# Performance work log

Hardware: AMD Instinct MI355X
Metric: run time of the kernel (lower is better)

Reference implementation:

```python
import jax, jax.numpy as jnp
import numpy as np

N_MEM = 50000
MATCH_THR2 = 0.01   # squared-distance match threshold (0.1 m)
EMA = 0.5           # EMA factor for matched-descriptor update
EPS = 1e-8


def _bilinear_depth(depth, uv):
    # depth: [H, W]; uv: [M, 2] pixel coords (u = x/col, v = y/row)
    H, W = depth.shape
    u = jnp.clip(uv[:, 0], 0.0, W - 1.001)
    v = jnp.clip(uv[:, 1], 0.0, H - 1.001)
    u0 = jnp.floor(u); v0 = jnp.floor(v)
    du = u - u0; dv = v - v0
    u0i = u0.astype(jnp.int32); v0i = v0.astype(jnp.int32)
    d00 = depth[v0i, u0i]
    d01 = depth[v0i, u0i + 1]
    d10 = depth[v0i + 1, u0i]
    d11 = depth[v0i + 1, u0i + 1]
    return d00 * (1 - du) * (1 - dv) + d01 * du * (1 - dv) + d10 * (1 - du) * dv + d11 * du * dv


def pix2world(points, depth_map, pose, K):
    # points [B,M,2], depth_map [B,1,H,W], pose [B,3,4] cam->world, K [B,3,3]
    d = jax.vmap(_bilinear_depth)(depth_map[:, 0], points)            # [B,M]
    pix = jnp.concatenate([points, jnp.ones_like(points[..., :1])], -1)  # [B,M,3]
    Kinv = jnp.linalg.inv(K)
    cam = jnp.einsum('bij,bmj->bmi', Kinv, pix) * d[..., None]        # [B,M,3]
    world = jnp.einsum('bij,bmj->bmi', pose[:, :, :3], cam) + pose[:, :, 3][:, None, :]
    valid = (d > 0) & jnp.isfinite(world).all(-1)                      # [B,M]
    return world, valid


def memory_write(pts, desc, valid, mem_pts, mem_desc, next_ptr):
    # pts [P,3], desc [P,D]; mem_pts [N,3], mem_desc [N,D]
    d2 = (jnp.sum(pts * pts, -1, keepdims=True)
          - 2.0 * pts @ mem_pts.T
          + jnp.sum(mem_pts * mem_pts, -1)[None, :])                  # [P,N]
    idx = jnp.argmin(d2, axis=1)                                       # [P]
    dmin = jnp.take_along_axis(d2, idx[:, None], axis=1)[:, 0]
    match = (dmin < MATCH_THR2) & valid
    n_match = match.sum()
    # returned descriptors come from the (non-differentiable) memory buffer;
    # unmatched entries return their own descriptor (cos=1 -> zero loss/grad)
    matched_desc = jax.lax.stop_gradient(jnp.where(match[:, None], mem_desc[idx], desc))
    # --- state update (buffers: no gradient) ---
    dsg = jax.lax.stop_gradient(desc)
    psg = jax.lax.stop_gradient(pts)
    unm = (~match) & valid
    slots = (next_ptr + jnp.cumsum(unm.astype(jnp.int32)) - 1) % N_MEM
    widx = jnp.where(unm, slots, idx)                                  # [P]
    old_pts = mem_pts[widx]; old_desc = mem_desc[widx]
    upd = old_desc * EMA + dsg * (1.0 - EMA)
    upd = upd / (jnp.linalg.norm(upd, axis=-1, keepdims=True) + EPS)
    new_desc_vals = jnp.where(match[:, None], upd, jnp.where(unm[:, None], dsg, old_desc))
    new_pts_vals = jnp.where(unm[:, None], psg, old_pts)
    new_mem_desc = mem_desc.at[widx].set(new_desc_vals)
    new_mem_pts = mem_pts.at[widx].set(new_pts_vals)
    return matched_desc, n_match, new_mem_pts, new_mem_desc


def setup_inputs() -> dict:
    key = jax.random.key(0)
    ks = jax.random.split(key, 8)
    B, M, D, H, W = 8, 512, 256, 480, 640
    points = jax.random.uniform(ks[0], (B, M, 2), jnp.float32) * jnp.array([W - 2.0, H - 2.0])
    depth_map = 0.5 + 4.5 * jax.random.uniform(ks[1], (B, 1, H, W), jnp.float32)
    # proper rotations via QR + small translations
    A = np.asarray(jax.random.normal(ks[2], (B, 3, 3)))
    Rs = np.stack([np.linalg.qr(A[b])[0] for b in range(B)]).astype(np.float32)
    t = np.asarray(jax.random.normal(ks[3], (B, 3, 1))) * 2.0
    pose = jnp.asarray(np.concatenate([Rs, t.astype(np.float32)], axis=2))  # [B,3,4]
    Kmat = jnp.broadcast_to(jnp.array([[320.0, 0.0, 320.0], [0.0, 320.0, 240.0], [0.0, 0.0, 1.0]], jnp.float32), (B, 3, 3))
    descriptors = jax.random.normal(ks[4], (B, M, D), jnp.float32)
    mem_pts = (jax.random.uniform(ks[5], (N_MEM, 3), jnp.float32) - 0.5) * 16.0
    mem_desc = jax.random.normal(ks[6], (N_MEM, D), jnp.float32)
    mem_desc = mem_desc / (jnp.linalg.norm(mem_desc, axis=-1, keepdims=True) + EPS)
    return {"points": points, "depth_map": depth_map, "pose": pose, "K": Kmat,
            "descriptors": descriptors, "mem_pts": mem_pts, "mem_desc": mem_desc,
            "next_ptr": 20000}


def reference(points, depth_map, pose, K, descriptors, mem_pts, mem_desc, next_ptr):
    world, valid = pix2world(points, depth_map, pose, K)               # [B,M,3], [B,M]
    P = world.shape[0] * world.shape[1]
    pts = world.reshape(P, 3)
    desc = descriptors.reshape(P, -1)
    vmask = valid.reshape(P)
    pts = jnp.where(vmask[:, None], pts, 1e6)   # invalid points never match
    matched_desc, n_match, new_mem_pts, new_mem_desc = memory_write(
        pts, desc, vmask, mem_pts, mem_desc, next_ptr)
    a = desc / jnp.maximum(jnp.linalg.norm(desc, axis=-1, keepdims=True), EPS)
    b = matched_desc / jnp.maximum(jnp.linalg.norm(matched_desc, axis=-1, keepdims=True), EPS)
    cos = jnp.sum(a * b, -1)                                           # [P]
    nv = jnp.maximum(vmask.sum(), 1)
    loss = 1.0 - jnp.sum(cos * vmask) / nv
    return loss, n_match, new_mem_pts, new_mem_desc
```

## Files before the change

### kernel.cpp

```cpp
#include <hip/hip_runtime.h>
#include <math.h>

#define N_MEM   50000
#define P_TOT   4096
#define DDIM    256
#define HDIM    480
#define WDIM    640
#define CHUNK   196
#define DISTB   1024
#define COPYB   512
#define THR2    0.01f
#define EPSF    1e-8f
typedef unsigned long long ull;

__device__ __forceinline__ unsigned fsort(float x) {
    unsigned b = __float_as_uint(x);
    return (b & 0x80000000u) ? ~b : (b | 0x80000000u);
}

__global__ void k_world(const float* __restrict__ points,
                        const float* __restrict__ depth,
                        const float* __restrict__ pose,
                        const float* __restrict__ Kmat,
                        float4* __restrict__ pts_out,
                        int* __restrict__ flags_out,
                        ull* __restrict__ minkey)
{
    int p = blockIdx.x * 256 + threadIdx.x;
    if (p >= P_TOT) return;
    minkey[p] = 0xFFFFFFFFFFFFFFFFULL;
    int b = p >> 9;
    const float* K = Kmat + b * 9;
    float a00=K[0],a01=K[1],a02=K[2],a10=K[3],a11=K[4],a12=K[5],a20=K[6],a21=K[7],a22=K[8];
    float det = a00*(a11*a22-a12*a21) - a01*(a10*a22-a12*a20) + a02*(a10*a21-a11*a20);
    float id = 1.0f/det;
    float i00=(a11*a22-a12*a21)*id, i01=(a02*a21-a01*a22)*id, i02=(a01*a12-a02*a11)*id;
    float i10=(a12*a20-a10*a22)*id, i11=(a00*a22-a02*a20)*id, i12=(a02*a10-a00*a12)*id;
    float i20=(a10*a21-a11*a20)*id, i21=(a01*a20-a00*a21)*id, i22=(a00*a11-a01*a10)*id;

    float u = points[p*2+0], v = points[p*2+1];
    float uc = fminf(fmaxf(u, 0.f), (float)WDIM - 1.001f);
    float vc = fminf(fmaxf(v, 0.f), (float)HDIM - 1.001f);
    float u0 = floorf(uc), v0 = floorf(vc);
    float du = uc - u0, dv = vc - v0;
    int u0i = (int)u0, v0i = (int)v0;
    const float* dm = depth + (size_t)b * HDIM * WDIM;
    float d00 = dm[v0i*WDIM + u0i];
    float d01 = dm[v0i*WDIM + u0i + 1];
    float d10 = dm[(v0i+1)*WDIM + u0i];
    float d11 = dm[(v0i+1)*WDIM + u0i + 1];
    float d = d00*(1.f-du)*(1.f-dv) + d01*du*(1.f-dv) + d10*(1.f-du)*dv + d11*du*dv;

    float cx = (i00*u + i01*v + i02) * d;
    float cy = (i10*u + i11*v + i12) * d;
    float cz = (i20*u + i21*v + i22) * d;
    const float* T = pose + b * 12;
    float wx = T[0]*cx + T[1]*cy + T[2]*cz  + T[3];
    float wy = T[4]*cx + T[5]*cy + T[6]*cz  + T[7];
    float wz = T[8]*cx + T[9]*cy + T[10]*cz + T[11];
    int val = (d > 0.f) && isfinite(wx) && isfinite(wy) && isfinite(wz);
    float4 o = val ? make_float4(wx, wy, wz, 0.f) : make_float4(1e6f, 1e6f, 1e6f, 0.f);
    pts_out[p] = o;
    flags_out[p] = val;
}

__global__ __launch_bounds__(256) void k_main(const float4* __restrict__ pts,
                                              const float* __restrict__ mem_pts,
                                              const float* __restrict__ mem_desc,
                                              ull* __restrict__ minkey,
                                              float* __restrict__ out_pts,
                                              float* __restrict__ out_desc)
{
    __shared__ float4 sm[CHUNK];
    int bid = blockIdx.x;
    int t = threadIdx.x;
    if (bid < DISTB) {
        int pb = bid >> 8;
        int ch = bid & 255;
        int j0 = ch * CHUNK;
        int cnt = min(CHUNK, N_MEM - j0);
        if (t < cnt) {
            float mx = mem_pts[(j0 + t) * 3 + 0];
            float my = mem_pts[(j0 + t) * 3 + 1];
            float mz = mem_pts[(j0 + t) * 3 + 2];
            sm[t] = make_float4(mx, my, mz, mx*mx + my*my + mz*mz);
        }
        __syncthreads();
        int p0 = pb * 1024 + t;
        float4 P0 = pts[p0], P1 = pts[p0+256], P2 = pts[p0+512], P3 = pts[p0+768];
        float pp0 = P0.x*P0.x + P0.y*P0.y + P0.z*P0.z;
        float pp1 = P1.x*P1.x + P1.y*P1.y + P1.z*P1.z;
        float pp2 = P2.x*P2.x + P2.y*P2.y + P2.z*P2.z;
        float pp3 = P3.x*P3.x + P3.y*P3.y + P3.z*P3.z;
        float bd0 = 3.4e38f, bd1 = 3.4e38f, bd2 = 3.4e38f, bd3 = 3.4e38f;
        int bi0 = 0, bi1 = 0, bi2 = 0, bi3 = 0;
        for (int j = 0; j < cnt; ++j) {
            float4 mv = sm[j];
            float dot0 = P0.x*mv.x + P0.y*mv.y + P0.z*mv.z;
            float dot1 = P1.x*mv.x + P1.y*mv.y + P1.z*mv.z;
            float dot2 = P2.x*mv.x + P2.y*mv.y + P2.z*mv.z;
            float dot3 = P3.x*mv.x + P3.y*mv.y + P3.z*mv.z;
            float d0 = pp0 - 2.f*dot0 + mv.w;
            float d1 = pp1 - 2.f*dot1 + mv.w;
            float d2 = pp2 - 2.f*dot2 + mv.w;
            float d3 = pp3 - 2.f*dot3 + mv.w;
            if (d0 < bd0) { bd0 = d0; bi0 = j0 + j; }
            if (d1 < bd1) { bd1 = d1; bi1 = j0 + j; }
            if (d2 < bd2) { bd2 = d2; bi2 = j0 + j; }
            if (d3 < bd3) { bd3 = d3; bi3 = j0 + j; }
        }
        atomicMin(&minkey[p0],       ((ull)fsort(bd0) << 32) | (unsigned)bi0);
        atomicMin(&minkey[p0 + 256], ((ull)fsort(bd1) << 32) | (unsigned)bi1);
        atomicMin(&minkey[p0 + 512], ((ull)fsort(bd2) << 32) | (unsigned)bi2);
        atomicMin(&minkey[p0 + 768], ((ull)fsort(bd3) << 32) | (unsigned)bi3);
    } else {
        const long tid = (long)(bid - DISTB) * 256 + t;
        const long stride = (long)COPYB * 256;
        const float2* ds = (const float2*)mem_desc;
        float2* dd = (float2*)out_desc;
        const long ND2 = (long)N_MEM * DDIM / 2;
        long k = tid * 4;
        const long stride4 = stride * 4;
        for (; k + 3 < ND2; k += stride4) {
            float2 a0 = ds[k+0], a1 = ds[k+1], a2 = ds[k+2], a3 = ds[k+3];
            dd[k+0] = a0; dd[k+1] = a1; dd[k+2] = a2; dd[k+3] = a3;
        }
        for (; k < ND2; ++k) dd[k] = ds[k];
        const float2* ps = (const float2*)mem_pts;
        float2* pd = (float2*)out_pts;
        for (long i = tid; i < (long)N_MEM * 3 / 2; i += stride) pd[i] = ps[i];
    }
}

__global__ __launch_bounds__(256) void k_scan(const ull* __restrict__ minkey,
                                              int* __restrict__ flags,
                                              const int* __restrict__ next_ptr,
                                              int* __restrict__ widx,
                                              int* __restrict__ winner,
                                              float* __restrict__ dout)
{
    __shared__ int su[256];
    __shared__ int smc[256];
    int t = threadIdx.x;
    int base = t * 16;
    const ull thr_key = ((ull)fsort(THR2)) << 32;
    int um[16], iv[16], wvv[16];
    int usum = 0, msum = 0;
    for (int k = 0; k < 16; k++) {
        ull key = minkey[base + k];
        int v = flags[base + k] & 1;
        int m = (key < thr_key) && v;
        int u = (!m) && v;
        iv[k] = (int)(key & 0xffffffffULL);
        um[k] = u; usum += u; msum += m;
        flags[base + k] = v | (m << 1) | (u << 2);
    }
    su[t] = usum; smc[t] = msum;
    __syncthreads();
    for (int off = 1; off < 256; off <<= 1) {
        int a = su[t], b = (t >= off) ? su[t - off] : 0;
        int c = smc[t], d = (t >= off) ? smc[t - off] : 0;
        __syncthreads();
        su[t] = a + b; smc[t] = c + d;
        __syncthreads();
    }
    int excl = su[t] - usum;
    int np_ = *next_ptr;
    int run = excl;
    for (int k = 0; k < 16; k++) {
        int wv;
        if (um[k]) { run += 1; wv = (np_ + run - 1) % N_MEM; }
        else       { wv = iv[k]; }
        widx[base + k] = wv;
        wvv[k] = wv;
        winner[wv] = -1;
    }
    __syncthreads();
    for (int k = 0; k < 16; k++)
        atomicMax(&winner[wvv[k]], base + k);
    if (t == 255) dout[1] = (float)smc[255];
}

__global__ __launch_bounds__(256) void k_scatloss(const int* __restrict__ widx,
                                                  const int* __restrict__ flags,
                                                  const int* __restrict__ winner,
                                                  const float* __restrict__ desc,
                                                  const float4* __restrict__ pts,
                                                  const float* __restrict__ mem_pts,
                                                  const float* __restrict__ mem_desc,
                                                  float* __restrict__ out_pts,
                                                  float* __restrict__ out_desc,
                                                  float* __restrict__ cos_ws)
{
    __shared__ float red[16];
    int p = blockIdx.x;
    int t = threadIdx.x;
    int f = flags[p];
    int v = f & 1, m = (f >> 1) & 1, u = (f >> 2) & 1;
    int wi = widx[p];
    int win = (winner[wi] == p);
    if (!m && !win) {
        if (t == 0) cos_ws[p] = v ? 1.f : 0.f;
        return;
    }
    float dsg = desc[p * DDIM + t];
    float old = mem_desc[(long)wi * DDIM + t];
    float val, cosv;
    if (m) {
        float up = old * 0.5f + dsg * 0.5f;
        float sdd = dsg * dsg, smm2 = old * old, sdm = dsg * old, suu = up * up;
        for (int off = 32; off; off >>= 1) {
            sdd  += __shfl_xor(sdd,  off);
            smm2 += __shfl_xor(smm2, off);
            sdm  += __shfl_xor(sdm,  off);
            suu  += __shfl_xor(suu,  off);
        }
        int w = t >> 6;
        if ((t & 63) == 0) { red[w] = sdd; red[4+w] = smm2; red[8+w] = sdm; red[12+w] = suu; }
        __syncthreads();
        float dd  = red[0] + red[1] + red[2] + red[3];
        float mm2 = red[4] + red[5] + red[6] + red[7];
        float dm  = red[8] + red[9] + red[10] + red[11];
        float uu  = red[12] + red[13] + red[14] + red[15];
        cosv = dm / (fmaxf(sqrtf(dd), EPSF) * fmaxf(sqrtf(mm2), EPSF));
        val = up / (sqrtf(uu) + EPSF);
    } else {
        cosv = v ? 1.f : 0.f;
        val = u ? dsg : old;
    }
    if (win) {
        out_desc[(long)wi * DDIM + t] = val;
        if (t == 0) {
            float px, py, pz;
            if (u) { float4 P = pts[p]; px = P.x; py = P.y; pz = P.z; }
            else   { px = mem_pts[wi*3]; py = mem_pts[wi*3+1]; pz = mem_pts[wi*3+2]; }
            out_pts[wi*3+0] = px; out_pts[wi*3+1] = py; out_pts[wi*3+2] = pz;
        }
    }
    if (t == 0) cos_ws[p] = cosv;
}

__global__ __launch_bounds__(256) void k_final(const float* __restrict__ cos_ws,
                                               const int* __restrict__ flags,
                                               float* __restrict__ dout)
{
    __shared__ float ss[256];
    __shared__ float sv[256];
    int t = threadIdx.x;
    float s = 0.f, v = 0.f;
    for (int k = t; k < P_TOT; k += 256) {
        s += cos_ws[k];
        v += (float)(flags[k] & 1);
    }
    ss[t] = s; sv[t] = v;
    __syncthreads();
    for (int off = 128; off; off >>= 1) {
        if (t < off) { ss[t] += ss[t + off]; sv[t] += sv[t + off]; }
        __syncthreads();
    }
    if (t == 0) {
        float nv = fmaxf(sv[0], 1.f);
        dout[0] = 1.f - ss[0] / nv;
    }
}

extern "C" void kernel_launch(void* const* d_in, const int* in_sizes, int n_in,
                              void* d_out, int out_size, void* d_ws, size_t ws_size,
                              hipStream_t stream)
{
    const float* points   = (const float*)d_in[0];
    const float* depth    = (const float*)d_in[1];
    const float* pose     = (const float*)d_in[2];
    const float* Kmat     = (const float*)d_in[3];
    const float* desc     = (const float*)d_in[4];
    const float* mem_pts  = (const float*)d_in[5];
    const float* mem_desc = (const float*)d_in[6];
    const int*   next_ptr = (const int*)d_in[7];

    float* out      = (float*)d_out;
    float* out_pts  = out + 2;
    float* out_desc = out + 2 + (long)N_MEM * 3;

    char* ws = (char*)d_ws;
    float4* pts_ws  = (float4*)(ws);
    int* flags_ws   = (int*)(ws + 65536);
    int* widx_ws    = (int*)(ws + 81920);
    int* winner_ws  = (int*)(ws + 98304);
    float* cos_ws   = (float*)(ws + 298304);
    ull* minkey_ws  = (ull*)(ws + 314688);

    k_world   <<<16, 256, 0, stream>>>(points, depth, pose, Kmat, pts_ws, flags_ws, minkey_ws);
    k_main    <<<DISTB + COPYB, 256, 0, stream>>>(pts_ws, mem_pts, mem_desc, minkey_ws,
                                                  out_pts, out_desc);
    k_scan    <<<1, 256, 0, stream>>>(minkey_ws, flags_ws, next_ptr,
                                      widx_ws, winner_ws, out);
    k_scatloss<<<P_TOT, 256, 0, stream>>>(widx_ws, flags_ws, winner_ws, desc, pts_ws,
                                          mem_pts, mem_desc, out_pts, out_desc, cos_ws);
    k_final   <<<1, 256, 0, stream>>>(cos_ws, flags_ws, out);
}
```

Baseline: 177.0 us.

## Interleave distance and copy blocks, read memory points directly without LDS staging

Blocks of the fused main kernel now alternate between nearest-neighbour distance work (even IDs) and descriptor/points copying (odd IDs). The copy now uses 1024 blocks instead of 512, so bandwidth-bound and compute-bound work share the CUs concurrently. The distance loop drops the shared-memory staging and __syncthreads. It reads mem_pts straight from global memory as uniform scalar-like loads and recomputes the squared norm per entry. Removing the barrier and LDS frees occupancy, but it adds a few extra FLOPs per candidate and relies on the cache for repeated loads.

```diff
diff --git a/kernel.cpp b/kernel.cpp
--- a/kernel.cpp
+++ b/kernel.cpp
@@ -7,8 +7,7 @@
 #define HDIM    480
 #define WDIM    640
 #define CHUNK   196
-#define DISTB   1024
-#define COPYB   512
+#define NPAIR   2048
 #define THR2    0.01f
 #define EPSF    1e-8f
 typedef unsigned long long ull;
@@ -71,21 +70,14 @@
                                               float* __restrict__ out_pts,
                                               float* __restrict__ out_desc)
 {
-    __shared__ float4 sm[CHUNK];
     int bid = blockIdx.x;
     int t = threadIdx.x;
-    if (bid < DISTB) {
-        int pb = bid >> 8;
-        int ch = bid & 255;
+    if ((bid & 1) == 0) {
+        int db = bid >> 1;
+        int pb = db >> 8;
+        int ch = db & 255;
         int j0 = ch * CHUNK;
         int cnt = min(CHUNK, N_MEM - j0);
-        if (t < cnt) {
-            float mx = mem_pts[(j0 + t) * 3 + 0];
-            float my = mem_pts[(j0 + t) * 3 + 1];
-            float mz = mem_pts[(j0 + t) * 3 + 2];
-            sm[t] = make_float4(mx, my, mz, mx*mx + my*my + mz*mz);
-        }
-        __syncthreads();
         int p0 = pb * 1024 + t;
         float4 P0 = pts[p0], P1 = pts[p0+256], P2 = pts[p0+512], P3 = pts[p0+768];
         float pp0 = P0.x*P0.x + P0.y*P0.y + P0.z*P0.z;
@@ -94,16 +86,21 @@
         float pp3 = P3.x*P3.x + P3.y*P3.y + P3.z*P3.z;
         float bd0 = 3.4e38f, bd1 = 3.4e38f, bd2 = 3.4e38f, bd3 = 3.4e38f;
         int bi0 = 0, bi1 = 0, bi2 = 0, bi3 = 0;
+        const float* mp = mem_pts + (long)j0 * 3;
+        #pragma unroll 4
         for (int j = 0; j < cnt; ++j) {
-            float4 mv = sm[j];
-            float dot0 = P0.x*mv.x + P0.y*mv.y + P0.z*mv.z;
-            float dot1 = P1.x*mv.x + P1.y*mv.y + P1.z*mv.z;
-            float dot2 = P2.x*mv.x + P2.y*mv.y + P2.z*mv.z;
-            float dot3 = P3.x*mv.x + P3.y*mv.y + P3.z*mv.z;
-            float d0 = pp0 - 2.f*dot0 + mv.w;
-            float d1 = pp1 - 2.f*dot1 + mv.w;
-            float d2 = pp2 - 2.f*dot2 + mv.w;
-            float d3 = pp3 - 2.f*dot3 + mv.w;
+            float mx = mp[j*3+0];
+            float my = mp[j*3+1];
+            float mz = mp[j*3+2];
+            float mm = mx*mx + my*my + mz*mz;
+            float dot0 = P0.x*mx + P0.y*my + P0.z*mz;
+            float dot1 = P1.x*mx + P1.y*my + P1.z*mz;
+            float dot2 = P2.x*mx + P2.y*my + P2.z*mz;
+            float dot3 = P3.x*mx + P3.y*my + P3.z*mz;
+            float d0 = pp0 - 2.f*dot0 + mm;
+            float d1 = pp1 - 2.f*dot1 + mm;
+            float d2 = pp2 - 2.f*dot2 + mm;
+            float d3 = pp3 - 2.f*dot3 + mm;
             if (d0 < bd0) { bd0 = d0; bi0 = j0 + j; }
             if (d1 < bd1) { bd1 = d1; bi1 = j0 + j; }
             if (d2 < bd2) { bd2 = d2; bi2 = j0 + j; }
@@ -114,8 +111,9 @@
         atomicMin(&minkey[p0 + 512], ((ull)fsort(bd2) << 32) | (unsigned)bi2);
         atomicMin(&minkey[p0 + 768], ((ull)fsort(bd3) << 32) | (unsigned)bi3);
     } else {
-        const long tid = (long)(bid - DISTB) * 256 + t;
-        const long stride = (long)COPYB * 256;
+        const long cb = bid >> 1;
+        const long tid = cb * 256 + t;
+        const long stride = (long)(NPAIR / 2) * 256;
         const float2* ds = (const float2*)mem_desc;
         float2* dd = (float2*)out_desc;
         const long ND2 = (long)N_MEM * DDIM / 2;
@@ -290,8 +288,8 @@
     ull* minkey_ws  = (ull*)(ws + 314688);
 
     k_world   <<<16, 256, 0, stream>>>(points, depth, pose, Kmat, pts_ws, flags_ws, minkey_ws);
-    k_main    <<<DISTB + COPYB, 256, 0, stream>>>(pts_ws, mem_pts, mem_desc, minkey_ws,
-                                                  out_pts, out_desc);
+    k_main    <<<NPAIR, 256, 0, stream>>>(pts_ws, mem_pts, mem_desc, minkey_ws,
+                                          out_pts, out_desc);
     k_scan    <<<1, 256, 0, stream>>>(minkey_ws, flags_ws, next_ptr,
                                       widx_ws, winner_ws, out);
     k_scatloss<<<P_TOT, 256, 0, stream>>>(widx_ws, flags_ws, winner_ws, desc, pts_ws,
```

Result: slower. 209.4 us (+18.4%).
